# Kernel tuning notes

Measured on AMD Instinct MI355X. Metric: run time of the kernel, lower is better.

## Reference

```python
import jax, jax.numpy as jnp
import numpy as np

N_CELLS = 50000
DEG = 32
NNZ = N_CELLS * DEG
D_IN = 64
D_OUT = 64
NEG_SLOPE = 0.2


def setup_inputs() -> dict:
    key = jax.random.key(0)
    k0, k1, k2, k3, k4 = jax.random.split(key, 5)
    x_source = jax.random.normal(k0, (N_CELLS, D_IN), jnp.float32)
    # COO indices of the sparse neighborhood matrix N: DEG entries per row
    edge_rows = jnp.repeat(jnp.arange(N_CELLS, dtype=jnp.int32), DEG)
    edge_cols = jax.random.randint(k1, (NNZ,), 0, N_CELLS, dtype=jnp.int32)
    neighborhood_values = jax.random.uniform(k2, (NNZ,), jnp.float32)
    # xavier_uniform-ish scales (exact init irrelevant for correctness baseline)
    W0 = jax.random.normal(k3, (D_IN, D_OUT), jnp.float32) * (1.414 / np.sqrt(D_IN))
    a0 = jax.random.normal(k4, (2 * D_OUT, 1), jnp.float32) * 0.1
    return {
        "x_source": x_source,
        "edge_rows": edge_rows,
        "edge_cols": edge_cols,
        "neighborhood_values": neighborhood_values,
        "W0": W0,
        "a0": a0,
    }


def reference(x_source, edge_rows, edge_cols, neighborhood_values, W0, a0):
    # message = X W_p  : [n_cells, d_out]
    message = x_source @ W0
    d = message.shape[1]
    # [X_i || X_j] a  ==  (X_i a_src) + (X_j a_dst); compute node-level dot first,
    # then gather per edge (avoids materializing [nnz, 2d] concat)
    a_src = a0[:d, 0]
    a_dst = a0[d:, 0]
    node_src = message @ a_src  # [n_cells]
    node_dst = message @ a_dst  # [n_cells]
    e = jax.nn.leaky_relu(node_src[edge_rows] + node_dst[edge_cols],
                          negative_slope=NEG_SLOPE)  # [nnz]
    # sparse_row_norm: divide each edge value by its row sum (softmax=False path)
    row_sum = jax.ops.segment_sum(e, edge_rows, num_segments=N_CELLS)
    att = e / row_sum[edge_rows]
    # Hadamard product N^1 \odot A_1, then SpMM with message
    vals = neighborhood_values * att  # [nnz]
    out = jax.ops.segment_sum(vals[:, None] * message[edge_cols], edge_rows,
                              num_segments=N_CELLS)  # [n_cells, d_out]
    # update_func='relu'
    return jax.nn.relu(out)
```

## Files before the change

### kernel.cpp

```cpp
#include <hip/hip_runtime.h>
#include <hip/hip_fp16.h>

#define N_CELLS 50000
#define DEG 32
#define DIM 64
#define NEG_SLOPE 0.2
#define NPAIRS (N_CELLS / 2)
#define NQUADS (N_CELLS / 4)

__global__ __launch_bounds__(256, 8)
void gat_prep(const float* __restrict__ x,
              const float* __restrict__ W0,
              const float* __restrict__ a0,
              __half* __restrict__ m2,
              double* __restrict__ ns,
              double* __restrict__ nd) {
  __shared__ double2 p_s[DIM];
  __shared__ float wl[DIM * DIM];
  __shared__ float x_s[4][4][DIM];

  const int tid = threadIdx.x;
  const int lane = tid & 63;
  const int wid = tid >> 6;

  {
    const float4* g4 = (const float4*)W0;
    float4* l4 = (float4*)wl;
#pragma unroll
    for (int i = 0; i < 4; ++i) l4[tid + i * 256] = g4[tid + i * 256];
  }

  if (tid < DIM) {
    double ps = 0.0, pd = 0.0;
    const float4* w4 = (const float4*)(W0 + (size_t)tid * DIM);
#pragma unroll
    for (int q = 0; q < DIM / 4; ++q) {
      float4 w = w4[q];
      ps = fma((double)w.x, (double)a0[4 * q + 0], ps);
      ps = fma((double)w.y, (double)a0[4 * q + 1], ps);
      ps = fma((double)w.z, (double)a0[4 * q + 2], ps);
      ps = fma((double)w.w, (double)a0[4 * q + 3], ps);
      pd = fma((double)w.x, (double)a0[DIM + 4 * q + 0], pd);
      pd = fma((double)w.y, (double)a0[DIM + 4 * q + 1], pd);
      pd = fma((double)w.z, (double)a0[DIM + 4 * q + 2], pd);
      pd = fma((double)w.w, (double)a0[DIM + 4 * q + 3], pd);
    }
    p_s[tid] = make_double2(ps, pd);
  }
  __syncthreads();

  {
    const int r = blockIdx.x * 256 + tid;
    if (r < N_CELLS) {
      const float4* x4 = (const float4*)(x + (size_t)r * DIM);
      double s0 = 0.0, s1 = 0.0, d0 = 0.0, d1 = 0.0;
#pragma unroll
      for (int q = 0; q < DIM / 4; ++q) {
        float4 v = x4[q];
        double2 p0 = p_s[4 * q + 0], p1 = p_s[4 * q + 1];
        double2 p2 = p_s[4 * q + 2], p3 = p_s[4 * q + 3];
        s0 = fma((double)v.x, p0.x, s0); d0 = fma((double)v.x, p0.y, d0);
        s1 = fma((double)v.y, p1.x, s1); d1 = fma((double)v.y, p1.y, d1);
        s0 = fma((double)v.z, p2.x, s0); d0 = fma((double)v.z, p2.y, d0);
        s1 = fma((double)v.w, p3.x, s1); d1 = fma((double)v.w, p3.y, d1);
      }
      ns[r] = s0 + s1;
      nd[r] = d0 + d1;
    }
  }

  const int gw = blockIdx.x * 4 + wid;
  const int nwv = gridDim.x * 4;
  const int rrow = lane >> 4;
  const int rcol = (lane & 15) * 4;

  for (int qi = gw; qi < NQUADS; qi += nwv) {
    const int r0 = qi * 4;
    *(float4*)&x_s[wid][rrow][rcol] =
        *(const float4*)(x + (size_t)(r0 + rrow) * DIM + rcol);

    float a0_ = 0.f, a1_ = 0.f, a2_ = 0.f, a3_ = 0.f;
    const float4* xr0 = (const float4*)x_s[wid][0];
    const float4* xr1 = (const float4*)x_s[wid][1];
    const float4* xr2 = (const float4*)x_s[wid][2];
    const float4* xr3 = (const float4*)x_s[wid][3];
#pragma unroll
    for (int q = 0; q < DIM / 4; ++q) {
      const float w0_ = wl[(4 * q + 0) * DIM + lane];
      const float w1_ = wl[(4 * q + 1) * DIM + lane];
      const float w2_ = wl[(4 * q + 2) * DIM + lane];
      const float w3_ = wl[(4 * q + 3) * DIM + lane];
      const float4 va = xr0[q];
      const float4 vb = xr1[q];
      const float4 vc = xr2[q];
      const float4 vd = xr3[q];
      a0_ = fmaf(va.x, w0_, a0_); a0_ = fmaf(va.y, w1_, a0_);
      a0_ = fmaf(va.z, w2_, a0_); a0_ = fmaf(va.w, w3_, a0_);
      a1_ = fmaf(vb.x, w0_, a1_); a1_ = fmaf(vb.y, w1_, a1_);
      a1_ = fmaf(vb.z, w2_, a1_); a1_ = fmaf(vb.w, w3_, a1_);
      a2_ = fmaf(vc.x, w0_, a2_); a2_ = fmaf(vc.y, w1_, a2_);
      a2_ = fmaf(vc.z, w2_, a2_); a2_ = fmaf(vc.w, w3_, a2_);
      a3_ = fmaf(vd.x, w0_, a3_); a3_ = fmaf(vd.y, w1_, a3_);
      a3_ = fmaf(vd.z, w2_, a3_); a3_ = fmaf(vd.w, w3_, a3_);
    }
    m2[(size_t)(r0 + 0) * DIM + lane] = __float2half(a0_);
    m2[(size_t)(r0 + 1) * DIM + lane] = __float2half(a1_);
    m2[(size_t)(r0 + 2) * DIM + lane] = __float2half(a2_);
    m2[(size_t)(r0 + 3) * DIM + lane] = __float2half(a3_);
  }
}

__global__ __launch_bounds__(256, 4)
void gat_edges(const __half* __restrict__ m2,
               const int* __restrict__ ecol,
               const float* __restrict__ nv,
               const double* __restrict__ ns,
               const double* __restrict__ nd,
               float* __restrict__ out) {
  __shared__ __align__(16) float w_s[4][2][DEG];
  __shared__ __align__(16) int c_s[4][2][DEG];

  const int lane = threadIdx.x & 63;
  const int wid = threadIdx.x >> 6;
  const int half = lane >> 5;
  const int sub = lane & 31;

  const int gwave = blockIdx.x * 4 + wid;
  const int nwaves = gridDim.x * 4;
  const unsigned* xp = (const unsigned*)m2;

  int col_c = 0; float nv_c = 0.0f; double nd_c = 0.0, ns_c = 0.0;
  if (gwave < NPAIRS) {
    const int eidx = 2 * gwave * DEG + lane;
    col_c = __builtin_nontemporal_load(ecol + eidx);
    nv_c = __builtin_nontemporal_load(nv + eidx);
    nd_c = nd[col_c];
    ns_c = ns[2 * gwave + half];
  }

  for (int p = gwave; p < NPAIRS; p += nwaves) {
    const int r0 = 2 * p;
    const float nvv = nv_c;
    const double z = ns_c + nd_c;

    c_s[wid][half][sub] = col_c;
    const int* cs = c_s[wid][half];
    unsigned pk[DEG];
#pragma unroll
    for (int i = 0; i < DEG; ++i)
      pk[i] = xp[(size_t)cs[i] * (DIM / 2) + sub];

    const int pn = p + nwaves;
    const int psafe = (pn < NPAIRS) ? pn : p;
    const int eidxn = 2 * psafe * DEG + lane;
    col_c = __builtin_nontemporal_load(ecol + eidxn);
    nv_c = __builtin_nontemporal_load(nv + eidxn);
    ns_c = ns[2 * psafe + half];

    double e = (z >= 0.0) ? z : NEG_SLOPE * z;
    double rs = e;
#pragma unroll
    for (int m = 16; m >= 1; m >>= 1) rs += __shfl_xor(rs, m, 64);
    w_s[wid][half][sub] = nvv * ((float)e / (float)rs);

    nd_c = nd[col_c];

    const float* wsp = w_s[wid][half];
    float ax = 0.0f, ay = 0.0f;
#pragma unroll
    for (int i = 0; i < DEG; ++i) {
      float2 v = __half22float2(*(const __half2*)&pk[i]);
      float w = wsp[i];
      ax = fmaf(w, v.x, ax);
      ay = fmaf(w, v.y, ay);
    }

    float2 o = make_float2(fmaxf(ax, 0.0f), fmaxf(ay, 0.0f));
    union { float2 f; unsigned long long u; } cv; cv.f = o;
    __builtin_nontemporal_store(
        cv.u, (unsigned long long*)(out + (size_t)(r0 + half) * DIM + 2 * sub));
  }
}

extern "C" void kernel_launch(void* const* d_in, const int* in_sizes, int n_in,
                              void* d_out, int out_size, void* d_ws, size_t ws_size,
                              hipStream_t stream) {
  const float* x = (const float*)d_in[0];
  const int* ecol = (const int*)d_in[2];
  const float* nv = (const float*)d_in[3];
  const float* W0 = (const float*)d_in[4];
  const float* a0 = (const float*)d_in[5];
  float* out = (float*)d_out;

  __half* m2 = (__half*)d_ws;
  double* ns = (double*)((char*)d_ws + (size_t)N_CELLS * DIM * sizeof(__half));
  double* nd = ns + N_CELLS;

  hipLaunchKernelGGL(gat_prep, dim3(1024), dim3(256), 0, stream,
                     x, W0, a0, m2, ns, nd);
  hipLaunchKernelGGL(gat_edges, dim3(2048), dim3(256), 0, stream,
                     m2, ecol, nv, ns, nd, out);
}
```

Baseline: 121.9 us.

## Fuse prep and edge kernels into one cooperative kernel with grid sync

Merges the node-projection/message kernel and the edge aggregation kernel into a single cooperative launch, separated by a grid-wide barrier, with grid size derived from the occupancy query and capped at 1024 blocks. It also preloads the first edge columns and values before the barrier so those loads overlap the wait. The aim is to remove the second launch and the inter-kernel gap. In exchange, the edge phase now runs on at most 1024 blocks instead of 2048 and loses the prep kernel's higher occupancy bound, and the grid sync adds its own cost.

New measurement: 214.6 us. 1.76x slower.

```diff
diff --git a/kernel.cpp b/kernel.cpp
--- a/kernel.cpp
+++ b/kernel.cpp
@@ -1,5 +1,8 @@
 #include <hip/hip_runtime.h>
 #include <hip/hip_fp16.h>
+#include <hip/hip_cooperative_groups.h>
+
+namespace cg = cooperative_groups;
 
 #define N_CELLS 50000
 #define DEG 32
@@ -8,20 +11,27 @@
 #define NPAIRS (N_CELLS / 2)
 #define NQUADS (N_CELLS / 4)
 
-__global__ __launch_bounds__(256, 8)
-void gat_prep(const float* __restrict__ x,
-              const float* __restrict__ W0,
-              const float* __restrict__ a0,
-              __half* __restrict__ m2,
-              double* __restrict__ ns,
-              double* __restrict__ nd) {
+__global__ __launch_bounds__(256, 4)
+void gat_fused(const float* __restrict__ x,
+               const int* __restrict__ ecol,
+               const float* __restrict__ nv,
+               const float* __restrict__ W0,
+               const float* __restrict__ a0,
+               __half* __restrict__ m2,
+               double* __restrict__ ns,
+               double* __restrict__ nd,
+               float* __restrict__ out) {
   __shared__ double2 p_s[DIM];
   __shared__ float wl[DIM * DIM];
   __shared__ float x_s[4][4][DIM];
+  __shared__ __align__(16) float w_s[4][2][DEG];
+  __shared__ __align__(16) int c_s[4][2][DEG];
 
   const int tid = threadIdx.x;
   const int lane = tid & 63;
   const int wid = tid >> 6;
+  const int half = lane >> 5;
+  const int sub = lane & 31;
 
   {
     const float4* g4 = (const float4*)W0;
@@ -49,24 +59,21 @@
   }
   __syncthreads();
 
-  {
-    const int r = blockIdx.x * 256 + tid;
-    if (r < N_CELLS) {
-      const float4* x4 = (const float4*)(x + (size_t)r * DIM);
-      double s0 = 0.0, s1 = 0.0, d0 = 0.0, d1 = 0.0;
-#pragma unroll
-      for (int q = 0; q < DIM / 4; ++q) {
-        float4 v = x4[q];
-        double2 p0 = p_s[4 * q + 0], p1 = p_s[4 * q + 1];
-        double2 p2 = p_s[4 * q + 2], p3 = p_s[4 * q + 3];
-        s0 = fma((double)v.x, p0.x, s0); d0 = fma((double)v.x, p0.y, d0);
-        s1 = fma((double)v.y, p1.x, s1); d1 = fma((double)v.y, p1.y, d1);
-        s0 = fma((double)v.z, p2.x, s0); d0 = fma((double)v.z, p2.y, d0);
-        s1 = fma((double)v.w, p3.x, s1); d1 = fma((double)v.w, p3.y, d1);
-      }
-      ns[r] = s0 + s1;
-      nd[r] = d0 + d1;
-    }
+  for (int r = blockIdx.x * 256 + tid; r < N_CELLS; r += gridDim.x * 256) {
+    const float4* x4 = (const float4*)(x + (size_t)r * DIM);
+    double s0 = 0.0, s1 = 0.0, d0 = 0.0, d1 = 0.0;
+#pragma unroll
+    for (int q = 0; q < DIM / 4; ++q) {
+      float4 v = x4[q];
+      double2 p0 = p_s[4 * q + 0], p1 = p_s[4 * q + 1];
+      double2 p2 = p_s[4 * q + 2], p3 = p_s[4 * q + 3];
+      s0 = fma((double)v.x, p0.x, s0); d0 = fma((double)v.x, p0.y, d0);
+      s1 = fma((double)v.y, p1.x, s1); d1 = fma((double)v.y, p1.y, d1);
+      s0 = fma((double)v.z, p2.x, s0); d0 = fma((double)v.z, p2.y, d0);
+      s1 = fma((double)v.w, p3.x, s1); d1 = fma((double)v.w, p3.y, d1);
+    }
+    ns[r] = s0 + s1;
+    nd[r] = d0 + d1;
   }
 
   const int gw = blockIdx.x * 4 + wid;
@@ -108,35 +115,19 @@
     m2[(size_t)(r0 + 2) * DIM + lane] = __float2half(a2_);
     m2[(size_t)(r0 + 3) * DIM + lane] = __float2half(a3_);
   }
-}
-
-__global__ __launch_bounds__(256, 4)
-void gat_edges(const __half* __restrict__ m2,
-               const int* __restrict__ ecol,
-               const float* __restrict__ nv,
-               const double* __restrict__ ns,
-               const double* __restrict__ nd,
-               float* __restrict__ out) {
-  __shared__ __align__(16) float w_s[4][2][DEG];
-  __shared__ __align__(16) int c_s[4][2][DEG];
-
-  const int lane = threadIdx.x & 63;
-  const int wid = threadIdx.x >> 6;
-  const int half = lane >> 5;
-  const int sub = lane & 31;
-
-  const int gwave = blockIdx.x * 4 + wid;
-  const int nwaves = gridDim.x * 4;
+
+  const int gwave = gw;
+  const int nwaves = nwv;
+  const int eidx0 = 2 * gwave * DEG + lane;
+  int col_c = __builtin_nontemporal_load(ecol + eidx0);
+  float nv_c = __builtin_nontemporal_load(nv + eidx0);
+
+  cg::this_grid().sync();
+
+  double nd_c = nd[col_c];
+  double ns_c = ns[2 * gwave + half];
+
   const unsigned* xp = (const unsigned*)m2;
-
-  int col_c = 0; float nv_c = 0.0f; double nd_c = 0.0, ns_c = 0.0;
-  if (gwave < NPAIRS) {
-    const int eidx = 2 * gwave * DEG + lane;
-    col_c = __builtin_nontemporal_load(ecol + eidx);
-    nv_c = __builtin_nontemporal_load(nv + eidx);
-    nd_c = nd[col_c];
-    ns_c = ns[2 * gwave + half];
-  }
 
   for (int p = gwave; p < NPAIRS; p += nwaves) {
     const int r0 = 2 * p;
@@ -196,8 +187,16 @@
   double* ns = (double*)((char*)d_ws + (size_t)N_CELLS * DIM * sizeof(__half));
   double* nd = ns + N_CELLS;
 
-  hipLaunchKernelGGL(gat_prep, dim3(1024), dim3(256), 0, stream,
-                     x, W0, a0, m2, ns, nd);
-  hipLaunchKernelGGL(gat_edges, dim3(2048), dim3(256), 0, stream,
-                     m2, ecol, nv, ns, nd, out);
+  int nb = 0;
+  hipError_t qerr =
+      hipOccupancyMaxActiveBlocksPerMultiprocessor(&nb, gat_fused, 256, 0);
+  if (qerr != hipSuccess || nb <= 0) nb = 4;
+  int grid = nb * 256;
+  if (grid > 1024) grid = 1024;
+
+  void* args[] = {(void*)&x,  (void*)&ecol, (void*)&nv, (void*)&W0,
+                  (void*)&a0, (void*)&m2,   (void*)&ns, (void*)&nd,
+                  (void*)&out};
+  hipLaunchCooperativeKernel((void*)gat_fused, dim3(grid), dim3(256), args, 0,
+                             stream);
 }
```
